# Optimization experiments

Measured on AMD Instinct MI355X. Metric: run time of the kernel, lower is better.

The kernel has to match this reference:

```python
import jax, jax.numpy as jnp
import numpy as np

N, D, H, O = 200000, 256, 256, 128


def _linear_params(key, fan_in, fan_out):
    # matches torch.nn.Linear default init: U(-1/sqrt(fan_in), 1/sqrt(fan_in))
    lim = 1.0 / np.sqrt(fan_in)
    kw, kb = jax.random.split(key)
    W = jax.random.uniform(kw, (fan_in, fan_out), minval=-lim, maxval=lim, dtype=jnp.float32)
    b = jax.random.uniform(kb, (fan_out,), minval=-lim, maxval=lim, dtype=jnp.float32)
    return W, b


def setup_inputs() -> dict:
    key = jax.random.key(0)
    ks = jax.random.split(key, 6)
    node_embeddings = jax.random.normal(ks[0], (N, D), dtype=jnp.float32)
    # adjacency_list keys: all < N so every key is 'valid'
    adj_keys = jax.random.randint(ks[1], (N,), 0, N, dtype=jnp.int64) if jax.config.jax_enable_x64 else jax.random.randint(ks[1], (N,), 0, N, dtype=jnp.int32)
    W1, b1 = _linear_params(ks[2], D, H)
    W2, b2 = _linear_params(ks[3], H, H)
    W3, b3 = _linear_params(ks[4], H, H)
    Wo, bo = _linear_params(ks[5], H, O)
    return {
        "node_embeddings": node_embeddings,
        "adj_keys": adj_keys,
        "W1": W1, "b1": b1,
        "W2": W2, "b2": b2,
        "W3": W3, "b3": b3,
        "Wo": Wo, "bo": bo,
    }


def reference(node_embeddings, adj_keys, W1, b1, W2, b2, W3, b3, Wo, bo):
    # --- aggregation path (faithful to the torch code's actual math) ---
    # All adj_keys are < N, so valid_indices == keys and the re-enumeration
    # `mapping` makes `indices` exactly arange(num_keys).
    indices = jnp.arange(adj_keys.shape[0])
    neighbors = node_embeddings[indices]              # [N, D] row gather
    # torch.mean(row, dim=0) on a 1-D row == scalar mean over features
    aggregated_embeddings = jnp.mean(neighbors, axis=1)  # [N]

    # --- dense 3-layer SAGE MLP + output projection ---
    x = jax.nn.relu(node_embeddings @ W1 + b1)        # [N, H]
    x = jax.nn.relu(x @ W2 + b2)                      # [N, H]
    x = jax.nn.relu(x @ W3 + b3)                      # [N, H]
    x = x @ Wo + bo                                   # [N, O]
    return (x, aggregated_embeddings)
```

## Files before the change

kernel.cpp:

```cpp
#include <hip/hip_runtime.h>
#include <hip/hip_bf16.h>
#include <cstdint>


#define N_ROWS 200000
#define O_DIM  128
#define ROWS   64
#define NTILES 3125
#define GRIDP  256

typedef short bf16x8 __attribute__((ext_vector_type(8)));
typedef float f32x4  __attribute__((ext_vector_type(4)));

__device__ __forceinline__ unsigned short rne_bf16(float f) {
  unsigned int u = __float_as_uint(f);
  u += 0x7FFFu + ((u >> 16) & 1u);
  return (unsigned short)(u >> 16);
}

__device__ __forceinline__ int swz(int b) { return b ^ (((b >> 9) & 7) << 4); }

__global__ __launch_bounds__(256) void prep_kernel(
    const float* __restrict__ W1, const float* __restrict__ W2,
    const float* __restrict__ W3, const float* __restrict__ Wo,
    unsigned short* __restrict__ wt) {
  const int b = blockIdx.x;
  const int t = threadIdx.x;
  if (b < 256) {
    wt[b * 256 + t] = rne_bf16(W1[t * 256 + b]);
  } else if (b < 512) {
    const int o = b - 256;
    wt[65536 + o * 256 + t] = rne_bf16(W2[t * 256 + o]);
  } else if (b < 768) {
    const int o = b - 512;
    wt[131072 + o * 256 + t] = rne_bf16(W3[t * 256 + o]);
  } else {
    const int o = b - 768;
    wt[196608 + o * 256 + t] = rne_bf16(Wo[t * 128 + o]);
  }
}

template <bool FILL>
__device__ __forceinline__ void half_mm(
    const unsigned short* __restrict__ wslot, const char* __restrict__ actb,
    bf16x8 bc[8][4], f32x4 acc[4], int wave, int lc, int quad) {
  const char* wb = (const char*)wslot;
#pragma unroll
  for (int ks = 0; ks < 8; ++ks) {
    const int k0 = ks * 32;
    const bf16x8 afr =
        *(const bf16x8*)(wb + swz((wave * 16 + lc) * 512 + k0 * 2 + 16 * quad));
    if (FILL) {
#pragma unroll
      for (int nb = 0; nb < 4; ++nb)
        bc[ks][nb] = *(const bf16x8*)(actb +
                       swz((nb * 16 + lc) * 512 + k0 * 2 + 16 * quad));
    }
#pragma unroll
    for (int nb = 0; nb < 4; ++nb)
      acc[nb] = __builtin_amdgcn_mfma_f32_16x16x32_bf16(afr, bc[ks][nb],
                                                        acc[nb], 0, 0, 0);
  }
}

__device__ __forceinline__ void layer_store_act(
    char* __restrict__ actb, const float* __restrict__ bias,
    f32x4 acc0[4], f32x4 acc1[4], int wave, int lc, int quad) {
#pragma unroll
  for (int h = 0; h < 2; ++h) {
    f32x4* acc = h ? acc1 : acc0;
    const int ch = h * 128 + wave * 16 + 4 * quad;
    const f32x4 bb = *(const f32x4*)(bias + ch);
#pragma unroll
    for (int nb = 0; nb < 4; ++nb) {
      f32x4 v = acc[nb] + bb;
#pragma unroll
      for (int j = 0; j < 4; ++j) v[j] = fmaxf(v[j], 0.f);
      const int r = nb * 16 + lc;
      ushort4 hq;
      hq.x = rne_bf16(v[0]); hq.y = rne_bf16(v[1]);
      hq.z = rne_bf16(v[2]); hq.w = rne_bf16(v[3]);
      *(ushort4*)(actb + swz(r * 512 + ch * 2)) = hq;
    }
  }
}

__global__ __launch_bounds__(512, 2) void sage_kernel(
    const float* __restrict__ E,
    const float* __restrict__ b1, const float* __restrict__ b2,
    const float* __restrict__ b3, const float* __restrict__ bo,
    const unsigned short* __restrict__ wts,
    float* __restrict__ out_x, float* __restrict__ out_agg) {
  __shared__ __align__(16) unsigned short act[16384];
  __shared__ __align__(16) unsigned short wbuf[2][32768];
  char* actb = (char*)act;

  const int t    = threadIdx.x;
  const int wave = t >> 6;
  const int lane = t & 63;
  const int lc   = lane & 15;
  const int quad = lane >> 4;

  auto stage_issue = [&](const unsigned short* wsrc, unsigned short* slot) {
#pragma unroll
    for (int rnd = 0; rnd < 8; ++rnd) {
      const int lds_rel = rnd * 8192 + wave * 1024 + lane * 16;
      __builtin_amdgcn_global_load_lds(
          (const unsigned int*)((const char*)wsrc + swz(lds_rel)),
          (unsigned int*)((char*)slot + rnd * 8192 + wave * 1024),
          16, 0, 0);
    }
  };

  bf16x8 bc[8][4];
  f32x4 acc0[4], acc1[4];

  int tile = blockIdx.x;
  stage_issue(wts, wbuf[0]);
  int sel = 1;

  for (;;) {
    const long row0 = (long)tile * ROWS;

    __syncthreads();

    {
      f32x4 st[8];
#pragma unroll
      for (int i = 0; i < 8; ++i)
        st[i] = *(const f32x4*)(E + (row0 + i * 8 + wave) * 256 + lane * 4);
#pragma unroll
      for (int i = 0; i < 8; ++i) {
        const int r = i * 8 + wave;
        ushort4 h;
        h.x = rne_bf16(st[i][0]); h.y = rne_bf16(st[i][1]);
        h.z = rne_bf16(st[i][2]); h.w = rne_bf16(st[i][3]);
        *(ushort4*)(actb + swz(r * 512 + lane * 8)) = h;
        float s = st[i][0] + st[i][1] + st[i][2] + st[i][3];
        s += __shfl_down(s, 32);
        s += __shfl_down(s, 16);
        s += __shfl_down(s, 8);
        s += __shfl_down(s, 4);
        s += __shfl_down(s, 2);
        s += __shfl_down(s, 1);
        if (lane == 0) out_agg[row0 + r] = s * (1.0f / 256.0f);
      }
    }
    __syncthreads();

    const unsigned short* wl = wts;
    const float* bias[3] = {b1, b2, b3};
#pragma unroll 1
    for (int L = 0; L < 3; ++L) {
      stage_issue(wl + 32768, wbuf[sel]);
#pragma unroll
      for (int nb = 0; nb < 4; ++nb) acc0[nb] = (f32x4){0.f, 0.f, 0.f, 0.f};
      half_mm<true>(wbuf[sel ^ 1], actb, bc, acc0, wave, lc, quad);
      __syncthreads();
      sel ^= 1;

      stage_issue(L < 2 ? wl + 65536 : wts + 196608, wbuf[sel]);
#pragma unroll
      for (int nb = 0; nb < 4; ++nb) acc1[nb] = (f32x4){0.f, 0.f, 0.f, 0.f};
      half_mm<false>(wbuf[sel ^ 1], actb, bc, acc1, wave, lc, quad);
      layer_store_act(actb, bias[L], acc0, acc1, wave, lc, quad);
      __syncthreads();
      sel ^= 1;
      wl += 65536;
    }

    const int nxt = tile + GRIDP;
    const bool has_next = nxt < NTILES;
    if (has_next) stage_issue(wts, wbuf[sel]);
#pragma unroll
    for (int nb = 0; nb < 4; ++nb) acc0[nb] = (f32x4){0.f, 0.f, 0.f, 0.f};
    half_mm<true>(wbuf[sel ^ 1], actb, bc, acc0, wave, lc, quad);
    sel ^= 1;
    {
      const int ch = wave * 16 + 4 * quad;
      const f32x4 bb = *(const f32x4*)(bo + ch);
#pragma unroll
      for (int nb = 0; nb < 4; ++nb) {
        f32x4 v = acc0[nb] + bb;
        const long gr = row0 + nb * 16 + lc;
        *(f32x4*)&out_x[gr * O_DIM + ch] = v;
      }
    }

    if (!has_next) break;
    tile = nxt;
  }
}

extern "C" void kernel_launch(void* const* d_in, const int* in_sizes, int n_in,
                              void* d_out, int out_size, void* d_ws, size_t ws_size,
                              hipStream_t stream) {
  const float* E  = (const float*)d_in[0];
  const float* W1 = (const float*)d_in[2];
  const float* b1 = (const float*)d_in[3];
  const float* W2 = (const float*)d_in[4];
  const float* b2 = (const float*)d_in[5];
  const float* W3 = (const float*)d_in[6];
  const float* b3 = (const float*)d_in[7];
  const float* Wo = (const float*)d_in[8];
  const float* bo = (const float*)d_in[9];

  float* out_x   = (float*)d_out;
  float* out_agg = out_x + (size_t)N_ROWS * O_DIM;
  unsigned short* wts = (unsigned short*)d_ws;

  prep_kernel<<<896, 256, 0, stream>>>(W1, W2, W3, Wo, wts);

  sage_kernel<<<GRIDP, 512, 0, stream>>>(E, b1, b2, b3, bo, wts, out_x, out_agg);
}
```

Measured before the change: 523.8 us.

## Keep hidden-layer weights in registers and prefetch embedding tiles into LDS

```diff
diff --git a/kernel.cpp b/kernel.cpp
--- a/kernel.cpp
+++ b/kernel.cpp
@@ -40,51 +40,6 @@
   }
 }
 
-template <bool FILL>
-__device__ __forceinline__ void half_mm(
-    const unsigned short* __restrict__ wslot, const char* __restrict__ actb,
-    bf16x8 bc[8][4], f32x4 acc[4], int wave, int lc, int quad) {
-  const char* wb = (const char*)wslot;
-#pragma unroll
-  for (int ks = 0; ks < 8; ++ks) {
-    const int k0 = ks * 32;
-    const bf16x8 afr =
-        *(const bf16x8*)(wb + swz((wave * 16 + lc) * 512 + k0 * 2 + 16 * quad));
-    if (FILL) {
-#pragma unroll
-      for (int nb = 0; nb < 4; ++nb)
-        bc[ks][nb] = *(const bf16x8*)(actb +
-                       swz((nb * 16 + lc) * 512 + k0 * 2 + 16 * quad));
-    }
-#pragma unroll
-    for (int nb = 0; nb < 4; ++nb)
-      acc[nb] = __builtin_amdgcn_mfma_f32_16x16x32_bf16(afr, bc[ks][nb],
-                                                        acc[nb], 0, 0, 0);
-  }
-}
-
-__device__ __forceinline__ void layer_store_act(
-    char* __restrict__ actb, const float* __restrict__ bias,
-    f32x4 acc0[4], f32x4 acc1[4], int wave, int lc, int quad) {
-#pragma unroll
-  for (int h = 0; h < 2; ++h) {
-    f32x4* acc = h ? acc1 : acc0;
-    const int ch = h * 128 + wave * 16 + 4 * quad;
-    const f32x4 bb = *(const f32x4*)(bias + ch);
-#pragma unroll
-    for (int nb = 0; nb < 4; ++nb) {
-      f32x4 v = acc[nb] + bb;
-#pragma unroll
-      for (int j = 0; j < 4; ++j) v[j] = fmaxf(v[j], 0.f);
-      const int r = nb * 16 + lc;
-      ushort4 hq;
-      hq.x = rne_bf16(v[0]); hq.y = rne_bf16(v[1]);
-      hq.z = rne_bf16(v[2]); hq.w = rne_bf16(v[3]);
-      *(ushort4*)(actb + swz(r * 512 + ch * 2)) = hq;
-    }
-  }
-}
-
 __global__ __launch_bounds__(512, 2) void sage_kernel(
     const float* __restrict__ E,
     const float* __restrict__ b1, const float* __restrict__ b2,
@@ -92,7 +47,8 @@
     const unsigned short* __restrict__ wts,
     float* __restrict__ out_x, float* __restrict__ out_agg) {
   __shared__ __align__(16) unsigned short act[16384];
-  __shared__ __align__(16) unsigned short wbuf[2][32768];
+  __shared__ __align__(16) unsigned short wo_l[32768];
+  __shared__ __align__(16) float est[16384];
   char* actb = (char*)act;
 
   const int t    = threadIdx.x;
@@ -101,34 +57,98 @@
   const int lc   = lane & 15;
   const int quad = lane >> 4;
 
-  auto stage_issue = [&](const unsigned short* wsrc, unsigned short* slot) {
+  bf16x8 wreg[3][2][8];
+#pragma unroll
+  for (int L = 0; L < 3; ++L)
+#pragma unroll
+    for (int mb = 0; mb < 2; ++mb)
+#pragma unroll
+      for (int ks = 0; ks < 8; ++ks)
+        wreg[L][mb][ks] = *(const bf16x8*)&wts[L * 65536 +
+            (wave * 32 + mb * 16 + lc) * 256 + ks * 32 + 8 * quad];
+#pragma unroll
+  for (int L = 0; L < 3; ++L)
+#pragma unroll
+    for (int mb = 0; mb < 2; ++mb)
+#pragma unroll
+      for (int ks = 0; ks < 8; ++ks)
+        asm volatile("" : "+v"(wreg[L][mb][ks]));
+
+  {
+    const char* wsrc = (const char*)(wts + 196608);
 #pragma unroll
     for (int rnd = 0; rnd < 8; ++rnd) {
-      const int lds_rel = rnd * 8192 + wave * 1024 + lane * 16;
+      const int rel = rnd * 8192 + wave * 1024 + lane * 16;
       __builtin_amdgcn_global_load_lds(
-          (const unsigned int*)((const char*)wsrc + swz(lds_rel)),
-          (unsigned int*)((char*)slot + rnd * 8192 + wave * 1024),
-          16, 0, 0);
+          (const unsigned int*)(wsrc + swz(rel)),
+          (unsigned int*)((char*)wo_l + rnd * 8192 + wave * 1024), 16, 0, 0);
+    }
+  }
+
+  auto stageE = [&](int tl) {
+    const char* src = (const char*)(E + (long)tl * ROWS * 256);
+#pragma unroll
+    for (int rnd = 0; rnd < 8; ++rnd) {
+      const int rel = rnd * 8192 + wave * 1024 + lane * 16;
+      __builtin_amdgcn_global_load_lds(
+          (const unsigned int*)(src + rel),
+          (unsigned int*)((char*)est + rnd * 8192 + wave * 1024), 16, 0, 0);
     }
   };
 
-  bf16x8 bc[8][4];
-  f32x4 acc0[4], acc1[4];
+  auto layer3 = [&](const bf16x8 (&wl)[2][8], const float* bias) {
+    f32x4 acc[2][4];
+#pragma unroll
+    for (int mb = 0; mb < 2; ++mb)
+#pragma unroll
+      for (int nb = 0; nb < 4; ++nb)
+        acc[mb][nb] = (f32x4){0.f, 0.f, 0.f, 0.f};
+#pragma unroll
+    for (int ks = 0; ks < 8; ++ks) {
+      bf16x8 bfr[4];
+#pragma unroll
+      for (int nb = 0; nb < 4; ++nb)
+        bfr[nb] = *(const bf16x8*)(actb +
+                     swz((nb * 16 + lc) * 512 + ks * 64 + 16 * quad));
+#pragma unroll
+      for (int mb = 0; mb < 2; ++mb)
+#pragma unroll
+        for (int nb = 0; nb < 4; ++nb)
+          acc[mb][nb] = __builtin_amdgcn_mfma_f32_16x16x32_bf16(
+              wl[mb][ks], bfr[nb], acc[mb][nb], 0, 0, 0);
+    }
+    __syncthreads();
+#pragma unroll
+    for (int mb = 0; mb < 2; ++mb) {
+      const int ch = wave * 32 + mb * 16 + 4 * quad;
+      const f32x4 bb = *(const f32x4*)(bias + ch);
+#pragma unroll
+      for (int nb = 0; nb < 4; ++nb) {
+        f32x4 v = acc[mb][nb] + bb;
+#pragma unroll
+        for (int j = 0; j < 4; ++j) v[j] = fmaxf(v[j], 0.f);
+        const int r = nb * 16 + lc;
+        ushort4 h;
+        h.x = rne_bf16(v[0]); h.y = rne_bf16(v[1]);
+        h.z = rne_bf16(v[2]); h.w = rne_bf16(v[3]);
+        *(ushort4*)(actb + swz(r * 512 + ch * 2)) = h;
+      }
+    }
+    __syncthreads();
+  };
 
   int tile = blockIdx.x;
-  stage_issue(wts, wbuf[0]);
-  int sel = 1;
+  stageE(tile);
 
   for (;;) {
     const long row0 = (long)tile * ROWS;
-
     __syncthreads();
 
     {
       f32x4 st[8];
 #pragma unroll
       for (int i = 0; i < 8; ++i)
-        st[i] = *(const f32x4*)(E + (row0 + i * 8 + wave) * 256 + lane * 4);
+        st[i] = *(const f32x4*)((const char*)est + (i * 8 + wave) * 1024 + lane * 16);
 #pragma unroll
       for (int i = 0; i < 8; ++i) {
         const int r = i * 8 + wave;
@@ -148,40 +168,37 @@
     }
     __syncthreads();
 
-    const unsigned short* wl = wts;
-    const float* bias[3] = {b1, b2, b3};
-#pragma unroll 1
-    for (int L = 0; L < 3; ++L) {
-      stage_issue(wl + 32768, wbuf[sel]);
-#pragma unroll
-      for (int nb = 0; nb < 4; ++nb) acc0[nb] = (f32x4){0.f, 0.f, 0.f, 0.f};
-      half_mm<true>(wbuf[sel ^ 1], actb, bc, acc0, wave, lc, quad);
-      __syncthreads();
-      sel ^= 1;
-
-      stage_issue(L < 2 ? wl + 65536 : wts + 196608, wbuf[sel]);
-#pragma unroll
-      for (int nb = 0; nb < 4; ++nb) acc1[nb] = (f32x4){0.f, 0.f, 0.f, 0.f};
-      half_mm<false>(wbuf[sel ^ 1], actb, bc, acc1, wave, lc, quad);
-      layer_store_act(actb, bias[L], acc0, acc1, wave, lc, quad);
-      __syncthreads();
-      sel ^= 1;
-      wl += 65536;
-    }
-
     const int nxt = tile + GRIDP;
     const bool has_next = nxt < NTILES;
-    if (has_next) stage_issue(wts, wbuf[sel]);
-#pragma unroll
-    for (int nb = 0; nb < 4; ++nb) acc0[nb] = (f32x4){0.f, 0.f, 0.f, 0.f};
-    half_mm<true>(wbuf[sel ^ 1], actb, bc, acc0, wave, lc, quad);
-    sel ^= 1;
+    if (has_next) stageE(nxt);
+
+    layer3(wreg[0], b1);
+    layer3(wreg[1], b2);
+    layer3(wreg[2], b3);
+
     {
+      f32x4 acc4[4];
+#pragma unroll
+      for (int nb = 0; nb < 4; ++nb) acc4[nb] = (f32x4){0.f, 0.f, 0.f, 0.f};
+#pragma unroll
+      for (int ks = 0; ks < 8; ++ks) {
+        const bf16x8 afr = *(const bf16x8*)((char*)wo_l +
+            swz((wave * 16 + lc) * 512 + ks * 64 + 16 * quad));
+        bf16x8 bfr[4];
+#pragma unroll
+        for (int nb = 0; nb < 4; ++nb)
+          bfr[nb] = *(const bf16x8*)(actb +
+                       swz((nb * 16 + lc) * 512 + ks * 64 + 16 * quad));
+#pragma unroll
+        for (int nb = 0; nb < 4; ++nb)
+          acc4[nb] = __builtin_amdgcn_mfma_f32_16x16x32_bf16(
+              afr, bfr[nb], acc4[nb], 0, 0, 0);
+      }
       const int ch = wave * 16 + 4 * quad;
       const f32x4 bb = *(const f32x4*)(bo + ch);
 #pragma unroll
       for (int nb = 0; nb < 4; ++nb) {
-        f32x4 v = acc0[nb] + bb;
+        f32x4 v = acc4[nb] + bb;
         const long gr = row0 + nb * 16 + lc;
         *(f32x4*)&out_x[gr * O_DIM + ch] = v;
       }
```

Result: slower. 549.4 us (+4.9%).
